# Kernel tuning notes

Hardware: AMD Instinct MI355X
Metric: run time of the kernel (lower is better)

Reference implementation:

```python
import jax, jax.numpy as jnp
from jax import lax
import numpy as np

C = 192      # dim
L = 2        # focal_level
T = 8        # num_frames
KS = (3, 5)  # kernel_size = focal_factor*k + focal_window
B, H, W = 32, 56, 56  # B = 4 clips * T frames


def _gelu(v):
    return jax.nn.gelu(v, approximate=False)  # torch nn.GELU (erf)


def _dwconv2d(x, w):
    # x: (B,C,H,W), w: (C,1,k,k) depthwise; odd k + SAME == padding k//2
    return lax.conv_general_dilated(x, w, (1, 1), 'SAME',
                                    feature_group_count=x.shape[1],
                                    dimension_numbers=('NCHW', 'OIHW', 'NCHW'))


def _conv1d(x, w):
    # x: (N,C,T), w: (Cout,Cin,k) dense conv1d, SAME padding
    return lax.conv_general_dilated(x, w, (1,), 'SAME',
                                    dimension_numbers=('NCH', 'OIH', 'NCH'))


def setup_inputs() -> dict:
    key = jax.random.key(0)
    ks = jax.random.split(key, 12)
    s = 0.02
    return {
        'x':   jax.random.normal(ks[0], (B, H, W, C), jnp.float32),
        'Wf':  jax.random.normal(ks[1], (C, 2 * C + L + 1), jnp.float32) * s,
        'bf':  jnp.zeros((2 * C + L + 1,), jnp.float32),
        'Wft': jax.random.normal(ks[2], (C, C + L + 1), jnp.float32) * s,
        'bft': jnp.zeros((C + L + 1,), jnp.float32),
        'fw0': jax.random.normal(ks[3], (C, 1, KS[0], KS[0]), jnp.float32) * s,
        'fw1': jax.random.normal(ks[4], (C, 1, KS[1], KS[1]), jnp.float32) * s,
        'tw0': jax.random.normal(ks[5], (C, C, KS[0]), jnp.float32) * s,
        'tw1': jax.random.normal(ks[6], (C, C, KS[1]), jnp.float32) * s,
        'Wh':  jax.random.normal(ks[7], (C, C), jnp.float32) * s,
        'bh':  jnp.zeros((C,), jnp.float32),
        'Wht': jax.random.normal(ks[8], (C, C), jnp.float32) * s,
        'bht': jnp.zeros((C,), jnp.float32),
        'Wp':  jax.random.normal(ks[9], (C, C), jnp.float32) * s,
        'bp':  jnp.zeros((C,), jnp.float32),
    }


def reference(x, Wf, bf, Wft, bft, fw0, fw1, tw0, tw1, Wh, bh, Wht, bht, Wp, bp):
    Bt, Hh, Ww, Cc = x.shape
    b = Bt // T
    # ---- temporal branch: (b t) h w c -> (b h w) t c
    xt = x.reshape(b, T, Hh, Ww, Cc).transpose(0, 2, 3, 1, 4).reshape(b * Hh * Ww, T, Cc)
    xt = (xt @ Wft + bft).transpose(0, 2, 1)          # (N, C+L+1, T)
    ctx_t, gates_t = xt[:, :Cc], xt[:, Cc:]
    ctx_all_t = jnp.zeros_like(ctx_t)
    for l, tw in enumerate((tw0, tw1)):
        ctx_t = _gelu(_conv1d(ctx_t, tw))
        ctx_all_t = ctx_all_t + ctx_t * gates_t[:, l:l + 1]
    ctx_all_t = ctx_all_t + _gelu(ctx_t.mean(2, keepdims=True)) * gates_t[:, L:]
    mod_t = jnp.einsum('nct,oc->not', ctx_all_t, Wht) + bht[None, :, None]  # h_temporal 1x1
    # (b h w) c t -> (b t) c h w
    mod_t = mod_t.reshape(b, Hh, Ww, Cc, T).transpose(0, 4, 3, 1, 2).reshape(Bt, Cc, Hh, Ww)
    # ---- spatial branch
    xs = (x @ Wf + bf).transpose(0, 3, 1, 2)           # (B, 2C+L+1, H, W)
    q, ctx, gates = xs[:, :Cc], xs[:, Cc:2 * Cc], xs[:, 2 * Cc:]
    ctx_all = jnp.zeros_like(ctx)
    for l, fw in enumerate((fw0, fw1)):
        ctx = _gelu(_dwconv2d(ctx, fw))
        ctx_all = ctx_all + ctx * gates[:, l:l + 1]
    ctx_all = ctx_all + _gelu(ctx.mean((2, 3), keepdims=True)) * gates[:, L:]
    mod = jnp.einsum('bchw,oc->bohw', ctx_all, Wh) + bh[None, :, None, None]  # h 1x1
    x_out = (q * mod * mod_t).transpose(0, 2, 3, 1)    # (B,H,W,C)
    return x_out @ Wp + bp
```

## Files before the change

kernel.cpp:

```cpp
#include <hip/hip_runtime.h>
#include <math.h>

#define CC    192
#define TT    8
#define HH    56
#define WWD   56
#define PP    3136
#define NTOK  100352
#define NSEQ  12544

typedef __attribute__((ext_vector_type(8))) short short8v;
typedef __attribute__((ext_vector_type(4))) float f32x4;
using u16 = unsigned short;

__device__ __forceinline__ float gelu_f(float v) {
  return 0.5f * v * (1.0f + erff(v * 0.70710678f));
}

__device__ __forceinline__ u16 bf16hi(float f) {
  unsigned u = __builtin_bit_cast(unsigned, f);
  u += 0x7fffu + ((u >> 16) & 1u);
  return (u16)(u >> 16);
}
__device__ __forceinline__ float bf2f(u16 h) {
  unsigned u = ((unsigned)h) << 16;
  return __builtin_bit_cast(float, u);
}

__device__ __forceinline__ void split4(float4 v, uint2* ph, uint2* pl) {
  float vv[4] = {v.x, v.y, v.z, v.w};
  u16 hh[4], ll[4];
  #pragma unroll
  for (int u = 0; u < 4; ++u) {
    hh[u] = bf16hi(vv[u]);
    ll[u] = bf16hi(vv[u] - bf2f(hh[u]));
  }
  *ph = make_uint2((unsigned)hh[0] | ((unsigned)hh[1] << 16),
                   (unsigned)hh[2] | ((unsigned)hh[3] << 16));
  *pl = make_uint2((unsigned)ll[0] | ((unsigned)ll[1] << 16),
                   (unsigned)ll[2] | ((unsigned)ll[3] << 16));
}

__global__ __launch_bounds__(256) void k_wsplit(const float* __restrict__ in,
    u16* __restrict__ hi, u16* __restrict__ lo, int K) {
  int idx = blockIdx.x * 256 + threadIdx.x;
  int total = CC * CC * K;
  if (idx >= total) return;
  int i = idx % CC;
  int rest = idx / CC;
  int o = rest % CC;
  int k = rest / CC;
  float f = in[(o * CC + i) * K + k];
  u16 h = bf16hi(f);
  hi[idx] = h;
  lo[idx] = bf16hi(f - bf2f(h));
}

__global__ __launch_bounds__(256) void k_wsplit_in(const float* __restrict__ Wf,
    const float* __restrict__ Wft, u16* __restrict__ hi, u16* __restrict__ lo) {
  int idx = blockIdx.x * 256 + threadIdx.x;
  if (idx >= 768 * CC) return;
  int k = idx % CC;
  int j = idx / CC;
  float f = 0.0f;
  if (j < 387) f = Wf[k * 387 + j];
  else if (j < 582) f = Wft[k * 195 + (j - 387)];
  u16 h = bf16hi(f);
  hi[idx] = h;
  lo[idx] = bf16hi(f - bf2f(h));
}

__global__ __launch_bounds__(256) void k_wsplit_d(const float* __restrict__ in,
    u16* __restrict__ hi, u16* __restrict__ lo) {
  int idx = blockIdx.x * 256 + threadIdx.x;
  if (idx >= CC * CC) return;
  float f = in[idx];
  u16 h = bf16hi(f);
  hi[idx] = h;
  lo[idx] = bf16hi(f - bf2f(h));
}

__global__ __launch_bounds__(256) void k_wsplit_t(const float* __restrict__ in,
    u16* __restrict__ hi, u16* __restrict__ lo) {
  int idx = blockIdx.x * 256 + threadIdx.x;
  if (idx >= CC * CC) return;
  int c = idx % CC;
  int o = idx / CC;
  float f = in[c * CC + o];
  u16 h = bf16hi(f);
  hi[idx] = h;
  lo[idx] = bf16hi(f - bf2f(h));
}

__global__ __launch_bounds__(256, 3) void k_in_mfma(const float* __restrict__ x,
    const u16* __restrict__ WIh, const u16* __restrict__ WIl,
    const float* __restrict__ bf, const float* __restrict__ bft,
    float* __restrict__ QS, float* __restrict__ CS, float* __restrict__ GS,
    float* __restrict__ CT, float* __restrict__ GT)
{
  __shared__ __align__(16) u16 xh[32 * 200];
  __shared__ __align__(16) u16 xl[32 * 200];
  const int tid  = threadIdx.x;
  const int lane = tid & 63;
  const int w    = tid >> 6;
  const int lrow = lane & 15;
  const int lk   = (lane >> 4) * 8;
  const int orow = (lane >> 4) * 4;
  const int tk0  = blockIdx.x * 32;
  const int jw0  = blockIdx.y * 320 + w * 80;

  #pragma unroll
  for (int it = 0; it < 6; ++it) {
    int idx = tid + it * 256;
    int tokl = idx / 48;
    int c = (idx - tokl * 48) * 4;
    float4 v = *(const float4*)(x + (size_t)(tk0 + tokl) * CC + c);
    split4(v, (uint2*)&xh[tokl * 200 + c], (uint2*)&xl[tokl * 200 + c]);
  }
  __syncthreads();

  f32x4 acc[5][2] = {};
  #pragma unroll
  for (int kb = 0; kb < 6; ++kb) {
    int k0 = kb * 32;
    short8v ah[5], al[5], bh[2], bl[2];
    #pragma unroll
    for (int r = 0; r < 5; ++r) {
      size_t aoff = (size_t)(jw0 + r * 16 + lrow) * 192 + k0 + lk;
      ah[r] = *(const short8v*)(WIh + aoff);
      al[r] = *(const short8v*)(WIl + aoff);
    }
    #pragma unroll
    for (int c = 0; c < 2; ++c) {
      int tokl = c * 16 + lrow;
      bh[c] = *(const short8v*)&xh[tokl * 200 + k0 + lk];
      bl[c] = *(const short8v*)&xl[tokl * 200 + k0 + lk];
    }
    #pragma unroll
    for (int r = 0; r < 5; ++r)
      #pragma unroll
      for (int c = 0; c < 2; ++c) {
        acc[r][c] = __builtin_amdgcn_mfma_f32_16x16x32_bf16(ah[r], bh[c], acc[r][c], 0, 0, 0);
        acc[r][c] = __builtin_amdgcn_mfma_f32_16x16x32_bf16(ah[r], bl[c], acc[r][c], 0, 0, 0);
        acc[r][c] = __builtin_amdgcn_mfma_f32_16x16x32_bf16(al[r], bh[c], acc[r][c], 0, 0, 0);
      }
  }

  #pragma unroll
  for (int c = 0; c < 2; ++c) {
    int tok = tk0 + c * 16 + lrow;
    int bb = tok / PP;
    int hw = tok - bb * PP;
    size_t ctbase = ((size_t)((bb >> 3) * PP + hw) * 8 + (size_t)(bb & 7));
    #pragma unroll
    for (int r = 0; r < 5; ++r) {
      int jb = jw0 + r * 16 + orow;
      #pragma unroll
      for (int u = 0; u < 4; ++u) {
        int j = jb + u;
        if (j >= 582) continue;
        float bias = (j < 387) ? bf[j] : bft[j - 387];
        float val = acc[r][c][u] + bias;
        if (j < 192)      QS[(size_t)tok * CC + j] = val;
        else if (j < 384) CS[(size_t)tok * CC + (j - 192)] = val;
        else if (j < 387) GS[(size_t)tok * 3 + (j - 384)] = val;
        else if (j < 579) CT[ctbase * CC + (j - 387)] = val;
        else              GT[ctbase * 3 + (j - 579)] = val;
      }
    }
  }
}

#define PADB 200
__global__ __launch_bounds__(256, 3) void k_t_mfma(
    const float* __restrict__ CT, const float* __restrict__ GT,
    const u16* __restrict__ W3h,
    const u16* __restrict__ W5h,
    const u16* __restrict__ WHh, const u16* __restrict__ WHl,
    const float* __restrict__ bht, float* __restrict__ MT)
{
  __shared__ __align__(16) u16 bufh[48 * PADB];
  __shared__ __align__(16) u16 bufl[48 * PADB];
  __shared__ float gbuf[96];

  const int tid  = threadIdx.x;
  const int lane = tid & 63;
  const int w    = tid >> 6;
  const int m0   = w * 48;
  const int lrow = lane & 15;
  const int lk   = (lane >> 4) * 8;
  const int orow = (lane >> 4) * 4;
  const int n0   = blockIdx.x * 4;

  if (tid < 96) gbuf[tid] = GT[(size_t)n0 * 24 + tid];

  for (int i = tid; i < 16 * 96; i += 256) {
    int hc = i / 96, j = i - hc * 96;
    int s = hc >> 2, which = hc & 3;
    int pc = s * 12 + ((which < 2) ? which : (8 + which));
    ((unsigned*)&bufh[pc * PADB])[j] = 0u;
    ((unsigned*)&bufl[pc * PADB])[j] = 0u;
  }

  {
    const float4* src = (const float4*)(CT + (size_t)n0 * 1536);
    #pragma unroll
    for (int it = 0; it < 6; ++it) {
      int idx = tid + it * 256;
      int e = idx * 4;
      int s = e / 1536;
      int r2 = e - s * 1536;
      int t = r2 / 192;
      int c = r2 - t * 192;
      float4 v = src[idx];
      int pc = s * 12 + 2 + t;
      split4(v, (uint2*)&bufh[pc * PADB + c], (uint2*)&bufl[pc * PADB + c]);
    }
  }
  __syncthreads();

  int pcolBase[2];
  #pragma unroll
  for (int c = 0; c < 2; ++c) {
    int col = c * 16 + lrow;
    pcolBase[c] = (col >> 3) * 12 + 2 + (col & 7);
  }

#define LOADA1(WH, OFF, KB, AH) { \
    _Pragma("unroll") for (int r = 0; r < 3; ++r) { \
      size_t aoff = ((size_t)((OFF) * 192 + m0 + r * 16 + lrow)) * 192 + (KB) * 32 + lk; \
      AH[r] = *(const short8v*)(WH + aoff); } }
#define LOADB_T(SH, KB, BH, BL) { \
    _Pragma("unroll") for (int c = 0; c < 2; ++c) { \
      int pc = pcolBase[c] + (SH); \
      BH[c] = *(const short8v*)&bufh[pc * PADB + (KB) * 32 + lk]; \
      BL[c] = *(const short8v*)&bufl[pc * PADB + (KB) * 32 + lk]; } }
#define MFMA4(AH, BH, BL, ACC) { \
    _Pragma("unroll") for (int r = 0; r < 3; ++r) \
      _Pragma("unroll") for (int c = 0; c < 2; ++c) { \
        ACC[r][c] = __builtin_amdgcn_mfma_f32_16x16x32_bf16(AH[r], BH[c], ACC[r][c], 0, 0, 0); \
        ACC[r][c] = __builtin_amdgcn_mfma_f32_16x16x32_bf16(AH[r], BL[c], ACC[r][c], 0, 0, 0); } }

  f32x4 acc[3][2] = {};
  #pragma unroll
  for (int off = 0; off < 3; ++off) {
    #pragma unroll
    for (int kb = 0; kb < 6; ++kb) {
      short8v ah[3], bh[2], bl[2];
      LOADA1(W3h, off, kb, ah);
      LOADB_T(off - 1, kb, bh, bl);
      MFMA4(ah, bh, bl, acc);
    }
  }
  __syncthreads();

  #pragma unroll
  for (int r = 0; r < 3; ++r) {
    int o = m0 + r * 16 + orow;
    #pragma unroll
    for (int c = 0; c < 2; ++c) {
      int pc = pcolBase[c];
      f32x4 a = acc[r][c];
      u16 hh[4], ll[4];
      #pragma unroll
      for (int u = 0; u < 4; ++u) {
        float c1v = gelu_f(a[u]);
        hh[u] = bf16hi(c1v);
        ll[u] = bf16hi(c1v - bf2f(hh[u]));
      }
      *(uint2*)&bufh[pc * PADB + o] =
          make_uint2((unsigned)hh[0] | ((unsigned)hh[1] << 16),
                     (unsigned)hh[2] | ((unsigned)hh[3] << 16));
      *(uint2*)&bufl[pc * PADB + o] =
          make_uint2((unsigned)ll[0] | ((unsigned)ll[1] << 16),
                     (unsigned)ll[2] | ((unsigned)ll[3] << 16));
    }
  }
  __syncthreads();

  f32x4 acc2[3][2] = {};
  #pragma unroll
  for (int off = 0; off < 5; ++off) {
    #pragma unroll
    for (int kb = 0; kb < 6; ++kb) {
      short8v ah[3], bh[2], bl[2];
      LOADA1(W5h, off, kb, ah);
      LOADB_T(off - 2, kb, bh, bl);
      MFMA4(ah, bh, bl, acc2);
    }
  }
  __syncthreads();

  #pragma unroll
  for (int r = 0; r < 3; ++r) {
    int o = m0 + r * 16 + orow;
    #pragma unroll
    for (int c = 0; c < 2; ++c) {
      int col = c * 16 + lrow;
      int pc = pcolBase[c];
      float g0 = gbuf[col * 3 + 0];
      float g1 = gbuf[col * 3 + 1];
      float g2 = gbuf[col * 3 + 2];
      f32x4 a = acc2[r][c];
      uint2 c1hv = *(const uint2*)&bufh[pc * PADB + o];
      uint2 c1lv = *(const uint2*)&bufl[pc * PADB + o];
      u16 c1h4[4] = {(u16)(c1hv.x & 0xffff), (u16)(c1hv.x >> 16),
                     (u16)(c1hv.y & 0xffff), (u16)(c1hv.y >> 16)};
      u16 c1l4[4] = {(u16)(c1lv.x & 0xffff), (u16)(c1lv.x >> 16),
                     (u16)(c1lv.y & 0xffff), (u16)(c1lv.y >> 16)};
      u16 hh[4], ll[4];
      #pragma unroll
      for (int u = 0; u < 4; ++u) {
        float cv = gelu_f(a[u]);
        float sm = cv;
        sm += __shfl_xor(sm, 1);
        sm += __shfl_xor(sm, 2);
        sm += __shfl_xor(sm, 4);
        float gm = gelu_f(sm * 0.125f);
        float c1full = bf2f(c1h4[u]) + bf2f(c1l4[u]);
        float av = c1full * g0 + cv * g1 + gm * g2;
        hh[u] = bf16hi(av);
        ll[u] = bf16hi(av - bf2f(hh[u]));
      }
      *(uint2*)&bufh[pc * PADB + o] =
          make_uint2((unsigned)hh[0] | ((unsigned)hh[1] << 16),
                     (unsigned)hh[2] | ((unsigned)hh[3] << 16));
      *(uint2*)&bufl[pc * PADB + o] =
          make_uint2((unsigned)ll[0] | ((unsigned)ll[1] << 16),
                     (unsigned)ll[2] | ((unsigned)ll[3] << 16));
    }
  }
  __syncthreads();

  f32x4 acc3[3][2] = {};
  #pragma unroll
  for (int kb = 0; kb < 6; ++kb) {
    short8v ah[3], al[3], bh[2], bl[2];
    #pragma unroll
    for (int r = 0; r < 3; ++r) {
      size_t aoff = ((size_t)(m0 + r * 16 + lrow)) * 192 + kb * 32 + lk;
      ah[r] = *(const short8v*)(WHh + aoff);
      al[r] = *(const short8v*)(WHl + aoff);
    }
    LOADB_T(0, kb, bh, bl);
    #pragma unroll
    for (int r = 0; r < 3; ++r)
      #pragma unroll
      for (int c = 0; c < 2; ++c) {
        acc3[r][c] = __builtin_amdgcn_mfma_f32_16x16x32_bf16(ah[r], bh[c], acc3[r][c], 0, 0, 0);
        acc3[r][c] = __builtin_amdgcn_mfma_f32_16x16x32_bf16(ah[r], bl[c], acc3[r][c], 0, 0, 0);
        acc3[r][c] = __builtin_amdgcn_mfma_f32_16x16x32_bf16(al[r], bh[c], acc3[r][c], 0, 0, 0);
      }
  }
#undef LOADA1
#undef LOADB_T
#undef MFMA4

  #pragma unroll
  for (int r = 0; r < 3; ++r) {
    int o = m0 + r * 16 + orow;
    float4 bb4 = *(const float4*)&bht[o];
    #pragma unroll
    for (int c = 0; c < 2; ++c) {
      int col = c * 16 + lrow;
      int n = n0 + (col >> 3);
      int t = col & 7;
      int bg = n / PP;
      int hw = n - bg * PP;
      size_t tk = (size_t)(bg * 8 + t) * PP + hw;
      f32x4 a = acc3[r][c];
      *(float4*)&MT[tk * CC + o] =
          make_float4(a[0] + bb4.x, a[1] + bb4.y, a[2] + bb4.z, a[3] + bb4.w);
    }
  }
}

__global__ __launch_bounds__(256) void k_dwf(const float* __restrict__ CTX,
    const float* __restrict__ GS, const float* __restrict__ fw0,
    const float* __restrict__ fw1, float* __restrict__ A0,
    float* __restrict__ GMpart)
{
  __shared__ __align__(16) float sctx[14 * 14 * 32];
  __shared__ __align__(16) float sc1[12 * 12 * 32];
  __shared__ float w3s[9 * 32];
  __shared__ float w5s[25 * 32];
  __shared__ float smean[256];
  const int tid  = threadIdx.x;
  const int tile = blockIdx.x;
  const int cgi  = blockIdx.y;
  const int bb   = blockIdx.z;
  const int ty0  = (tile / 7) * 8;
  const int tx0  = (tile % 7) * 8;
  const int c0   = cgi * 32;

  for (int i = tid; i < 288; i += 256) {
    int k = i / 32, c = i - (i / 32) * 32;
    w3s[k * 32 + c] = fw0[(c0 + c) * 9 + k];
  }
  for (int i = tid; i < 800; i += 256) {
    int k = i / 32, c = i - (i / 32) * 32;
    w5s[k * 32 + c] = fw1[(c0 + c) * 25 + k];
  }

  for (int i = tid; i < 1568; i += 256) {
    int tok = i >> 3;
    int part = i & 7;
    int y = tok / 14, x = tok - y * 14;
    int gh = ty0 + y - 3, gw = tx0 + x - 3;
    float4 v = make_float4(0.f, 0.f, 0.f, 0.f);
    if (gh >= 0 && gh < HH && gw >= 0 && gw < WWD)
      v = *(const float4*)(CTX + ((size_t)bb * PP + gh * WWD + gw) * CC + c0 + part * 4);
    *(float4*)&sctx[tok * 32 + part * 4] = v;
  }
  __syncthreads();

  for (int i = tid; i < 4608; i += 256) {
    int c = i & 31, tok = i >> 5;
    int y = tok / 12, x = tok - y * 12;
    float s = 0.f;
    #pragma unroll
    for (int dy = 0; dy < 3; ++dy)
      #pragma unroll
      for (int dx = 0; dx < 3; ++dx)
        s = fmaf(sctx[((y + dy) * 14 + (x + dx)) * 32 + c], w3s[(dy * 3 + dx) * 32 + c], s);
    sc1[tok * 32 + c] = gelu_f(s);
  }
  __syncthreads();

  float ms = 0.f;
  #pragma unroll
  for (int p = 0; p < 8; ++p) {
    int i = tid + p * 256;
    int c = i & 31, tok = i >> 5;
    int y = tok >> 3, x = tok & 7;
    float s = 0.f;
    #pragma unroll
    for (int dy = 0; dy < 5; ++dy)
      #pragma unroll
      for (int dx = 0; dx < 5; ++dx)
        s = fmaf(sc1[((y + dy) * 12 + (x + dx)) * 32 + c], w5s[(dy * 5 + dx) * 32 + c], s);
    float c2 = gelu_f(s);
    ms += c2;
    float c1v = sc1[((y + 2) * 12 + (x + 2)) * 32 + c];
    size_t tg = (size_t)bb * PP + (size_t)(ty0 + y) * WWD + (tx0 + x);
    float g0 = GS[tg * 3 + 0];
    float g1 = GS[tg * 3 + 1];
    A0[tg * CC + c0 + c] = c1v * g0 + c2 * g1;
  }
  smean[tid] = ms;
  __syncthreads();
  if (tid < 32) {
    float s = 0.f;
    #pragma unroll
    for (int p = 0; p < 8; ++p) s += smean[p * 32 + tid];
    GMpart[(size_t)tile * 6144 + bb * CC + c0 + tid] = s;
  }
}

__global__ __launch_bounds__(256) void k_gmg(const float* __restrict__ GMpart,
                                             float* __restrict__ GMg)
{
  int i = blockIdx.x * 256 + threadIdx.x;
  if (i >= 6144) return;
  float s = 0.f;
  for (int p = 0; p < 49; ++p) s += GMpart[(size_t)p * 6144 + i];
  GMg[i] = gelu_f(s * (1.0f / 3136.0f));
}

__global__ __launch_bounds__(256, 3) void k_modout(float* __restrict__ A0,
    const float* __restrict__ GS, const float* __restrict__ GMg,
    const u16* __restrict__ Wmh, const u16* __restrict__ Wml,
    const float* __restrict__ bh, const float* __restrict__ QS,
    float* MTout, const u16* __restrict__ Wph, const u16* __restrict__ Wpl,
    const float* __restrict__ bp)
{
  __shared__ __align__(16) u16 sh_[32 * 200];
  __shared__ __align__(16) u16 sl_[32 * 200];
  const int tid  = threadIdx.x;
  const int lane = tid & 63;
  const int w    = tid >> 6;
  const int lrow = lane & 15;
  const int lk   = (lane >> 4) * 8;
  const int orow = (lane >> 4) * 4;
  const int tk0  = blockIdx.x * 32;
  const int m0   = w * 48;

  #pragma unroll
  for (int it = 0; it < 6; ++it) {
    int idx = tid + it * 256;
    int tokl = idx / 48;
    int c = (idx - tokl * 48) * 4;
    int tok = tk0 + tokl;
    int bb = tok / PP;
    size_t base = (size_t)tok * CC + c;
    float4 v1 = *(const float4*)(A0 + base);
    float4 vg = *(const float4*)(GMg + bb * CC + c);
    float g2 = GS[(size_t)tok * 3 + 2];
    float4 av = make_float4(v1.x + vg.x * g2, v1.y + vg.y * g2,
                            v1.z + vg.z * g2, v1.w + vg.w * g2);
    split4(av, (uint2*)&sh_[tokl * 200 + c], (uint2*)&sl_[tokl * 200 + c]);
  }
  __syncthreads();

#define LOADA_G(WH, WL, KB, AH, AL) { \
    _Pragma("unroll") for (int r = 0; r < 3; ++r) { \
      size_t aoff = (size_t)(m0 + r * 16 + lrow) * 192 + (KB) * 32 + lk; \
      AH[r] = *(const short8v*)(WH + aoff); \
      AL[r] = *(const short8v*)(WL + aoff); } }
#define LOADB_G(KB, BH, BL) { \
    _Pragma("unroll") for (int c = 0; c < 2; ++c) { \
      int tokl = c * 16 + lrow; \
      BH[c] = *(const short8v*)&sh_[tokl * 200 + (KB) * 32 + lk]; \
      BL[c] = *(const short8v*)&sl_[tokl * 200 + (KB) * 32 + lk]; } }
#define GEMM6(WH, WL, ACC) { \
    _Pragma("unroll") for (int kb = 0; kb < 6; ++kb) { \
      short8v ah[3], al[3], bh4[2], bl4[2]; \
      LOADA_G(WH, WL, kb, ah, al); \
      LOADB_G(kb, bh4, bl4); \
      _Pragma("unroll") for (int r = 0; r < 3; ++r) \
        _Pragma("unroll") for (int c = 0; c < 2; ++c) { \
          ACC[r][c] = __builtin_amdgcn_mfma_f32_16x16x32_bf16(ah[r], bh4[c], ACC[r][c], 0, 0, 0); \
          ACC[r][c] = __builtin_amdgcn_mfma_f32_16x16x32_bf16(ah[r], bl4[c], ACC[r][c], 0, 0, 0); \
          ACC[r][c] = __builtin_amdgcn_mfma_f32_16x16x32_bf16(al[r], bh4[c], ACC[r][c], 0, 0, 0); } } }

  f32x4 acc[3][2] = {};
  GEMM6(Wmh, Wml, acc);
  __syncthreads();

  #pragma unroll
  for (int r = 0; r < 3; ++r) {
    int jb = m0 + r * 16 + orow;
    float4 b4 = *(const float4*)&bh[jb];
    #pragma unroll
    for (int c = 0; c < 2; ++c) {
      int tokl = c * 16 + lrow;
      f32x4 a = acc[r][c];
      float4 mv = make_float4(a[0] + b4.x, a[1] + b4.y, a[2] + b4.z, a[3] + b4.w);
      split4(mv, (uint2*)&sh_[tokl * 200 + jb], (uint2*)&sl_[tokl * 200 + jb]);
    }
  }
  __syncthreads();

  #pragma unroll
  for (int it = 0; it < 6; ++it) {
    int idx = tid + it * 256;
    int tokl = idx / 48;
    int c = (idx - tokl * 48) * 4;
    size_t base = (size_t)(tk0 + tokl) * CC + c;
    float4 q  = *(const float4*)(QS + base);
    float4 mt = *(const float4*)(MTout + base);
    uint2 mh = *(const uint2*)&sh_[tokl * 200 + c];
    uint2 ml = *(const uint2*)&sl_[tokl * 200 + c];
    float m0v = bf2f((u16)(mh.x & 0xffff)) + bf2f((u16)(ml.x & 0xffff));
    float m1v = bf2f((u16)(mh.x >> 16))    + bf2f((u16)(ml.x >> 16));
    float m2v = bf2f((u16)(mh.y & 0xffff)) + bf2f((u16)(ml.y & 0xffff));
    float m3v = bf2f((u16)(mh.y >> 16))    + bf2f((u16)(ml.y >> 16));
    float4 av = make_float4(q.x * m0v * mt.x, q.y * m1v * mt.y,
                            q.z * m2v * mt.z, q.w * m3v * mt.w);
    split4(av, (uint2*)&sh_[tokl * 200 + c], (uint2*)&sl_[tokl * 200 + c]);
  }
  __syncthreads();

  f32x4 acc2[3][2] = {};
  GEMM6(Wph, Wpl, acc2);
#undef LOADA_G
#undef LOADB_G
#undef GEMM6

  #pragma unroll
  for (int r = 0; r < 3; ++r) {
    int jb = m0 + r * 16 + orow;
    float4 b4 = *(const float4*)&bp[jb];
    #pragma unroll
    for (int c = 0; c < 2; ++c) {
      int tok = tk0 + c * 16 + lrow;
      f32x4 a = acc2[r][c];
      *(float4*)&MTout[(size_t)tok * CC + jb] =
          make_float4(a[0] + b4.x, a[1] + b4.y, a[2] + b4.z, a[3] + b4.w);
    }
  }
}

extern "C" void kernel_launch(void* const* d_in, const int* in_sizes, int n_in,
                              void* d_out, int out_size, void* d_ws, size_t ws_size,
                              hipStream_t stream)
{
  (void)in_sizes; (void)n_in; (void)out_size; (void)ws_size;
  const float* x   = (const float*)d_in[0];
  const float* Wf  = (const float*)d_in[1];
  const float* bf  = (const float*)d_in[2];
  const float* Wft = (const float*)d_in[3];
  const float* bft = (const float*)d_in[4];
  const float* fw0 = (const float*)d_in[5];
  const float* fw1 = (const float*)d_in[6];
  const float* tw0 = (const float*)d_in[7];
  const float* tw1 = (const float*)d_in[8];
  const float* Wh  = (const float*)d_in[9];
  const float* bh  = (const float*)d_in[10];
  const float* Wht = (const float*)d_in[11];
  const float* bht = (const float*)d_in[12];
  const float* Wp  = (const float*)d_in[13];
  const float* bp  = (const float*)d_in[14];

  float* ws = (float*)d_ws;
  const size_t SZ = (size_t)NTOK * CC;
  float* QS     = ws + 0 * SZ;
  float* WS1    = ws + 1 * SZ;
  float* WS2    = ws + 2 * SZ;
  float* MT     = (float*)d_out;
  float* GS     = ws + 3 * SZ;
  float* GT     = GS + (size_t)NTOK * 3;
  float* GMpart = GT + (size_t)NTOK * 3;
  float* GMg    = GMpart + 49 * 6144;
  u16* W3h = (u16*)(GMg + 6144);
  u16* W3l = W3h + 3 * 36864;
  u16* W5h = W3l + 3 * 36864;
  u16* W5l = W5h + 5 * 36864;
  u16* WHh = W5l + 5 * 36864;
  u16* WHl = WHh + 36864;
  u16* WIh = WHl + 36864;
  u16* WIl = WIh + 768 * 192;
  u16* Wmh = WIl + 768 * 192;
  u16* Wml = Wmh + 36864;
  u16* Wph = Wml + 36864;
  u16* Wpl = Wph + 36864;

  k_wsplit<<<432, 256, 0, stream>>>(tw0, W3h, W3l, 3);
  k_wsplit<<<720, 256, 0, stream>>>(tw1, W5h, W5l, 5);
  k_wsplit<<<144, 256, 0, stream>>>(Wht, WHh, WHl, 1);
  k_wsplit_in<<<576, 256, 0, stream>>>(Wf, Wft, WIh, WIl);
  k_wsplit_d<<<144, 256, 0, stream>>>(Wh, Wmh, Wml);
  k_wsplit_t<<<144, 256, 0, stream>>>(Wp, Wph, Wpl);

  k_in_mfma<<<dim3(3136, 2), 256, 0, stream>>>(x, WIh, WIl, bf, bft,
                                               QS, WS1, GS, WS2, GT);
  k_t_mfma<<<3136, 256, 0, stream>>>(WS2, GT, W3h, W5h, WHh, WHl, bht, MT);

  k_dwf<<<dim3(49, 6, 32), 256, 0, stream>>>(WS1, GS, fw0, fw1, WS2, GMpart);
  k_gmg<<<24, 256, 0, stream>>>(GMpart, GMg);

  k_modout<<<3136, 256, 0, stream>>>(WS2, GS, GMg, Wmh, Wml, bh,
                                     QS, MT, Wph, Wpl, bp);
}
```

Measured before the change: 967.1 us.

## Fuse temporal MFMA and spatial depthwise kernels into one interleaved launch

Merges the temporal-branch MFMA kernel and the spatial depthwise-conv kernel into a single launch. Blocks are interleaved one temporal to three spatial so compute-heavy and memory-heavy work share the GPU at the same time. The spatial output goes to a new workspace buffer so it no longer overwrites the temporal input, which removes the ordering dependency. The fused path is taken only when the workspace is large enough; it costs extra workspace memory, and the combined kernel now uses the larger shared-memory footprint and a launch bound of 3 blocks for the depthwise part.

```diff
diff --git a/kernel.cpp b/kernel.cpp
--- a/kernel.cpp
+++ b/kernel.cpp
@@ -172,16 +172,15 @@
 }
 
 #define PADB 200
-__global__ __launch_bounds__(256, 3) void k_t_mfma(
+__device__ __forceinline__ void t_body(char* smem, int tblk,
     const float* __restrict__ CT, const float* __restrict__ GT,
-    const u16* __restrict__ W3h,
-    const u16* __restrict__ W5h,
+    const u16* __restrict__ W3h, const u16* __restrict__ W5h,
     const u16* __restrict__ WHh, const u16* __restrict__ WHl,
     const float* __restrict__ bht, float* __restrict__ MT)
 {
-  __shared__ __align__(16) u16 bufh[48 * PADB];
-  __shared__ __align__(16) u16 bufl[48 * PADB];
-  __shared__ float gbuf[96];
+  u16* bufh = (u16*)smem;
+  u16* bufl = bufh + 48 * PADB;
+  float* gbuf = (float*)(bufl + 48 * PADB);
 
   const int tid  = threadIdx.x;
   const int lane = tid & 63;
@@ -190,7 +189,7 @@
   const int lrow = lane & 15;
   const int lk   = (lane >> 4) * 8;
   const int orow = (lane >> 4) * 4;
-  const int n0   = blockIdx.x * 4;
+  const int n0   = tblk * 4;
 
   if (tid < 96) gbuf[tid] = GT[(size_t)n0 * 24 + tid];
 
@@ -375,20 +374,17 @@
   }
 }
 
-__global__ __launch_bounds__(256) void k_dwf(const float* __restrict__ CTX,
-    const float* __restrict__ GS, const float* __restrict__ fw0,
-    const float* __restrict__ fw1, float* __restrict__ A0,
-    float* __restrict__ GMpart)
-{
-  __shared__ __align__(16) float sctx[14 * 14 * 32];
-  __shared__ __align__(16) float sc1[12 * 12 * 32];
-  __shared__ float w3s[9 * 32];
-  __shared__ float w5s[25 * 32];
-  __shared__ float smean[256];
+__device__ __forceinline__ void dwf_body(char* smem, int tile, int cgi, int bb,
+    const float* __restrict__ CTX, const float* __restrict__ GS,
+    const float* __restrict__ fw0, const float* __restrict__ fw1,
+    float* __restrict__ A0, float* __restrict__ GMpart)
+{
+  float* sctx  = (float*)smem;
+  float* sc1   = sctx + 6272;
+  float* w3s   = sc1 + 4608;
+  float* w5s   = w3s + 288;
+  float* smean = w5s + 800;
   const int tid  = threadIdx.x;
-  const int tile = blockIdx.x;
-  const int cgi  = blockIdx.y;
-  const int bb   = blockIdx.z;
   const int ty0  = (tile / 7) * 8;
   const int tx0  = (tile % 7) * 8;
   const int c0   = cgi * 32;
@@ -454,6 +450,48 @@
     #pragma unroll
     for (int p = 0; p < 8; ++p) s += smean[p * 32 + tid];
     GMpart[(size_t)tile * 6144 + bb * CC + c0 + tid] = s;
+  }
+}
+
+__global__ __launch_bounds__(256, 3) void k_t_mfma(
+    const float* __restrict__ CT, const float* __restrict__ GT,
+    const u16* __restrict__ W3h, const u16* __restrict__ W5h,
+    const u16* __restrict__ WHh, const u16* __restrict__ WHl,
+    const float* __restrict__ bht, float* __restrict__ MT)
+{
+  __shared__ __align__(16) char smem[48896];
+  t_body(smem, blockIdx.x, CT, GT, W3h, W5h, WHh, WHl, bht, MT);
+}
+
+__global__ __launch_bounds__(256) void k_dwf(const float* __restrict__ CTX,
+    const float* __restrict__ GS, const float* __restrict__ fw0,
+    const float* __restrict__ fw1, float* __restrict__ A0,
+    float* __restrict__ GMpart)
+{
+  __shared__ __align__(16) char smem[48896];
+  dwf_body(smem, blockIdx.x, blockIdx.y, blockIdx.z, CTX, GS, fw0, fw1, A0, GMpart);
+}
+
+__global__ __launch_bounds__(256, 3) void k_fused(
+    const float* __restrict__ CT, const float* __restrict__ GT,
+    const u16* __restrict__ W3h, const u16* __restrict__ W5h,
+    const u16* __restrict__ WHh, const u16* __restrict__ WHl,
+    const float* __restrict__ bht, float* __restrict__ MT,
+    const float* __restrict__ CTX, const float* __restrict__ GS,
+    const float* __restrict__ fw0, const float* __restrict__ fw1,
+    float* __restrict__ A0, float* __restrict__ GMpart)
+{
+  __shared__ __align__(16) char smem[48896];
+  const int bid = blockIdx.x;
+  if ((bid & 3) == 0) {
+    t_body(smem, bid >> 2, CT, GT, W3h, W5h, WHh, WHl, bht, MT);
+  } else {
+    int s = bid - (bid >> 2) - 1;
+    int tile = s % 49;
+    int rest = s / 49;
+    int cgi = rest % 6;
+    int bb = rest / 6;
+    dwf_body(smem, tile, cgi, bb, CTX, GS, fw0, fw1, A0, GMpart);
   }
 }
 
@@ -585,7 +623,7 @@
                               void* d_out, int out_size, void* d_ws, size_t ws_size,
                               hipStream_t stream)
 {
-  (void)in_sizes; (void)n_in; (void)out_size; (void)ws_size;
+  (void)in_sizes; (void)n_in; (void)out_size;
   const float* x   = (const float*)d_in[0];
   const float* Wf  = (const float*)d_in[1];
   const float* bf  = (const float*)d_in[2];
@@ -624,6 +662,9 @@
   u16* Wml = Wmh + 36864;
   u16* Wph = Wml + 36864;
   u16* Wpl = Wph + 36864;
+  float* WS3 = (float*)(Wpl + 36864);
+  size_t need_bytes = (size_t)((char*)(WS3 + SZ) - (char*)d_ws);
+  const bool fused_ok = (ws_size >= need_bytes);
 
   k_wsplit<<<432, 256, 0, stream>>>(tw0, W3h, W3l, 3);
   k_wsplit<<<720, 256, 0, stream>>>(tw1, W5h, W5l, 5);
@@ -634,11 +675,18 @@
 
   k_in_mfma<<<dim3(3136, 2), 256, 0, stream>>>(x, WIh, WIl, bf, bft,
                                                QS, WS1, GS, WS2, GT);
-  k_t_mfma<<<3136, 256, 0, stream>>>(WS2, GT, W3h, W5h, WHh, WHl, bht, MT);
-
-  k_dwf<<<dim3(49, 6, 32), 256, 0, stream>>>(WS1, GS, fw0, fw1, WS2, GMpart);
-  k_gmg<<<24, 256, 0, stream>>>(GMpart, GMg);
-
-  k_modout<<<3136, 256, 0, stream>>>(WS2, GS, GMg, Wmh, Wml, bh,
-                                     QS, MT, Wph, Wpl, bp);
-}
+
+  if (fused_ok) {
+    k_fused<<<12544, 256, 0, stream>>>(WS2, GT, W3h, W5h, WHh, WHl, bht, MT,
+                                       WS1, GS, fw0, fw1, WS3, GMpart);
+    k_gmg<<<24, 256, 0, stream>>>(GMpart, GMg);
+    k_modout<<<3136, 256, 0, stream>>>(WS3, GS, GMg, Wmh, Wml, bh,
+                                       QS, MT, Wph, Wpl, bp);
+  } else {
+    k_t_mfma<<<3136, 256, 0, stream>>>(WS2, GT, W3h, W5h, WHh, WHl, bht, MT);
+    k_dwf<<<dim3(49, 6, 32), 256, 0, stream>>>(WS1, GS, fw0, fw1, WS2, GMpart);
+    k_gmg<<<24, 256, 0, stream>>>(GMpart, GMg);
+    k_modout<<<3136, 256, 0, stream>>>(WS2, GS, GMg, Wmh, Wml, bh,
+                                       QS, MT, Wph, Wpl, bp);
+  }
+}
```

Measured after the change: 996.5 us. 1.03x slower.
